# Kernel optimization log

Hardware: AMD Instinct MI355X
Metric: run time of the kernel (lower is better)

The kernel has to match this reference:

```python
import jax, jax.numpy as jnp
import numpy as np

N_NODES = 50000
N_EDGES = 800000
N_GRAPHS = 64
HIDDEN = 64


def setup_inputs() -> dict:
    key = jax.random.key(0)
    ks = jax.random.split(key, 16)
    inp = {
        "x": jax.random.normal(ks[0], (N_NODES, 1), dtype=jnp.float32),
        "edge_attr": jax.random.normal(ks[1], (N_EDGES, 1), dtype=jnp.float32),
        "edge_index": jax.random.randint(ks[2], (2, N_EDGES), 0, N_NODES, dtype=jnp.int32),
        "batch": jnp.sort(jax.random.randint(ks[3], (N_NODES,), 0, N_GRAPHS, dtype=jnp.int32)),
        # node/edge encoders: Linear(1, H)
        "W_node": jax.random.normal(ks[4], (1, HIDDEN), dtype=jnp.float32) * 0.1,
        "b_node": jnp.zeros((HIDDEN,), dtype=jnp.float32),
        "W_edge": jax.random.normal(ks[5], (1, HIDDEN), dtype=jnp.float32) * 0.1,
        "b_edge": jnp.zeros((HIDDEN,), dtype=jnp.float32),
        # message MLP: Linear(2H, H) + ReLU
        "W_msg": jax.random.normal(ks[6], (2 * HIDDEN, HIDDEN), dtype=jnp.float32) * (1.0 / np.sqrt(2 * HIDDEN)),
        "b_msg": jnp.zeros((HIDDEN,), dtype=jnp.float32),
        # update MLP: Linear(H, H) + ReLU
        "W_upd": jax.random.normal(ks[7], (HIDDEN, HIDDEN), dtype=jnp.float32) * (1.0 / np.sqrt(HIDDEN)),
        "b_upd": jnp.zeros((HIDDEN,), dtype=jnp.float32),
        # output: Linear(H, 1)
        "W_out": jax.random.normal(ks[8], (HIDDEN, 1), dtype=jnp.float32) * (1.0 / np.sqrt(HIDDEN)),
        "b_out": jnp.zeros((1,), dtype=jnp.float32),
    }
    return inp


def reference(x, edge_attr, edge_index, batch,
              W_node, b_node, W_edge, b_edge,
              W_msg, b_msg, W_upd, b_upd, W_out, b_out):
    # encoders
    h = x @ W_node + b_node                       # [N, H]
    e = edge_attr @ W_edge + b_edge               # [E, H]

    src, dst = edge_index[0], edge_index[1]
    x_j = h[src]                                  # gather source node feats [E, H]
    m = jax.nn.relu(jnp.concatenate([x_j, e], axis=-1) @ W_msg + b_msg)  # [E, H]

    # scatter-add aggregate to target nodes
    aggr = jax.ops.segment_sum(m, dst, num_segments=N_NODES)             # [N, H]

    # update MLP (applied to every node)
    upd = jax.nn.relu(aggr @ W_upd + b_upd)       # [N, H]

    # global mean pool per graph
    sums = jax.ops.segment_sum(upd, batch, num_segments=N_GRAPHS)        # [G, H]
    counts = jax.ops.segment_sum(jnp.ones((upd.shape[0],), dtype=upd.dtype), batch, num_segments=N_GRAPHS)
    avg = sums / jnp.maximum(counts, 1.0)[:, None]                       # [G, H]

    out = (avg @ W_out + b_out).squeeze(-1)       # [G]
    return out
```

## Files before the change

### kernel.cpp

```cpp
#include <hip/hip_runtime.h>

#define N_NODES 50000
#define N_EDGES 800000
#define N_GRAPHS 64
#define H 64
#define BN 64
#define NB ((N_NODES + BN - 1) / BN)
#define NGRP 8
#define CAPG 224
#define BSTRIDE (NGRP * CAPG)
#define CSTRIDE 16
#define CHUNK 4096
#define BINTHREADS 1024
#define EPT (CHUNK / BINTHREADS)
#define NCHUNK ((N_EDGES + CHUNK - 1) / CHUNK)

#define VALS_OFF  0
#define ABC_OFF   (NB * BSTRIDE * 2)
#define ZERO_OFF  (ABC_OFF + 3 * H)
#define GSUM_OFF  (ZERO_OFF)
#define GCNT_OFF  (GSUM_OFF + N_GRAPHS)
#define BCUR_OFF  (GCNT_OFF + N_GRAPHS)
#define ZERO_BYTES ((2 * N_GRAPHS + NGRP * NB * CSTRIDE) * 4)

__global__ __launch_bounds__(BINTHREADS) void k_bin(
    const float* __restrict__ x, const float* __restrict__ ea,
    const int* __restrict__ ei, int* __restrict__ bcur,
    float2* __restrict__ vals, float* __restrict__ abc,
    const float* __restrict__ Wn, const float* __restrict__ bn,
    const float* __restrict__ We, const float* __restrict__ be,
    const float* __restrict__ Wm, const float* __restrict__ bm)
{
    __shared__ int lh[NB], lbase[NB], lcur[NB];
    const int t = threadIdx.x;
    const int g = blockIdx.x & (NGRP - 1);
    for (int b = t; b < NB; b += BINTHREADS) { lh[b] = 0; lcur[b] = 0; }

    const int e0 = blockIdx.x * CHUNK;
    const int* __restrict__ src = ei;
    const int* __restrict__ dst = ei + N_EDGES;

    int   d[EPT];
    float xv[EPT], ev[EPT];
    bool  ok[EPT];
    #pragma unroll
    for (int k = 0; k < EPT; ++k) {
        const int e = e0 + t + k * BINTHREADS;
        ok[k] = (e < N_EDGES);
        const int ee = ok[k] ? e : (N_EDGES - 1);
        const int s  = src[ee];
        d[k]  = dst[ee];
        ev[k] = ea[ee];
        xv[k] = x[s];
    }
    __syncthreads();

    #pragma unroll
    for (int k = 0; k < EPT; ++k)
        if (ok[k]) atomicAdd(&lh[d[k] >> 6], 1);
    __syncthreads();

    for (int b = t; b < NB; b += BINTHREADS) {
        const int v = lh[b];
        if (v) lbase[b] = atomicAdd(&bcur[(g * NB + b) * CSTRIDE], v);
    }
    __syncthreads();

    #pragma unroll
    for (int k = 0; k < EPT; ++k) {
        if (ok[k]) {
            const int b  = d[k] >> 6;
            const int lp = atomicAdd(&lcur[b], 1);
            const int p  = lbase[b] + lp;
            if (p < CAPG) {
                const unsigned uy = (__float_as_uint(ev[k]) & 0xFFFFFFC0u) |
                                    (unsigned)(d[k] & (BN - 1));
                vals[b * BSTRIDE + g * CAPG + p] =
                    make_float2(xv[k], __uint_as_float(uy));
            }
        }
    }

    if (blockIdx.x == 0 && t < H) {
        const int k = t;
        float a = 0.f, b = 0.f, c = 0.f;
        #pragma unroll
        for (int i = 0; i < H; ++i) {
            float wt = Wm[i * H + k];
            float wb = Wm[(H + i) * H + k];
            a = fmaf(Wn[i], wt, a);
            b = fmaf(We[i], wb, b);
            c = fmaf(bn[i], wt, c);
            c = fmaf(be[i], wb, c);
        }
        abc[k]         = a;
        abc[H + k]     = b;
        abc[2 * H + k] = c + bm[k];
    }
}

__global__ __launch_bounds__(256) void k_fused(
    const float2* __restrict__ vals, const int* __restrict__ bcur,
    const float* __restrict__ abc, const float* __restrict__ Wu,
    const float* __restrict__ bu, const float* __restrict__ Wo,
    const int* __restrict__ batch,
    float* __restrict__ gsum, float* __restrict__ gcnt)
{
    __shared__ float2 stB[BSTRIDE];
    __shared__ int lh[BN], le[BN], lc[BN];
    __shared__ __align__(16) float sA[4][72];
    __shared__ float lsum[N_GRAPHS], lcnt[N_GRAPHS];

    const int t    = threadIdx.x;
    const int lane = t & 63;
    const int w    = t >> 6;
    const int b    = blockIdx.x;
    const int base = b * BSTRIDE;

    const float A   = abc[lane];
    const float B   = abc[H + lane];
    const float C   = abc[2 * H + lane];
    const float bul = bu[lane];
    const float wol = Wo[lane];
    float wr[64];
    #pragma unroll
    for (int i = 0; i < 64; ++i) wr[i] = Wu[i * H + lane];

    if (t < BN) lh[t] = 0;
    if (t < N_GRAPHS) { lsum[t] = 0.f; lcnt[t] = 0.f; }
    __syncthreads();

    int mg[NGRP];
    #pragma unroll
    for (int g = 0; g < NGRP; ++g) {
        const int v = bcur[(g * NB + b) * CSTRIDE];
        mg[g] = v < CAPG ? v : CAPG;
    }

    float2 r[NGRP];
    #pragma unroll
    for (int g = 0; g < NGRP; ++g) {
        if (t < mg[g]) {
            r[g] = vals[base + g * CAPG + t];
            atomicAdd(&lh[__float_as_uint(r[g].y) & (BN - 1)], 1);
        }
    }
    __syncthreads();

    if (t < BN) {
        const int v = lh[t];
        int incl = v;
        #pragma unroll
        for (int d = 1; d < BN; d <<= 1) {
            const int up = __shfl_up(incl, d);
            if (lane >= d) incl += up;
        }
        le[t] = incl - v;
        lc[t] = incl - v;
    }
    __syncthreads();

    #pragma unroll
    for (int g = 0; g < NGRP; ++g) {
        if (t < mg[g]) {
            const int rk = atomicAdd(&lc[__float_as_uint(r[g].y) & (BN - 1)], 1);
            stB[rk] = r[g];
        }
    }
    __syncthreads();

    #define MSG(q) fmaxf(fmaf((q).x, A, fmaf((q).y, B, C)), 0.f)
    for (int qn = 0; qn < BN / 4; ++qn) {
        const int ln   = w * (BN / 4) + qn;
        const int node = b * BN + ln;
        const int off  = le[ln];
        const int c    = lh[ln];

        float s0 = 0.f, s1 = 0.f, s2 = 0.f, s3 = 0.f;
        int j = 0;
        for (; j + 8 <= c; j += 8) {
            const float2 q0 = stB[off + j + 0], q1 = stB[off + j + 1];
            const float2 q2 = stB[off + j + 2], q3 = stB[off + j + 3];
            const float2 q4 = stB[off + j + 4], q5 = stB[off + j + 5];
            const float2 q6 = stB[off + j + 6], q7 = stB[off + j + 7];
            s0 += MSG(q0); s1 += MSG(q1); s2 += MSG(q2); s3 += MSG(q3);
            s0 += MSG(q4); s1 += MSG(q5); s2 += MSG(q6); s3 += MSG(q7);
        }
        for (; j < c; ++j) { const float2 q = stB[off + j]; s0 += MSG(q); }
        const float s = (s0 + s1) + (s2 + s3);

        sA[w][lane] = s;
        float t0 = 0.f, t1 = 0.f, t2 = 0.f, t3 = 0.f;
        #pragma unroll
        for (int i = 0; i < 64; i += 4) {
            const float4 av = *(const float4*)&sA[w][i];
            t0 = fmaf(av.x, wr[i + 0], t0);
            t1 = fmaf(av.y, wr[i + 1], t1);
            t2 = fmaf(av.z, wr[i + 2], t2);
            t3 = fmaf(av.w, wr[i + 3], t3);
        }
        const float tk = (t0 + t1) + (t2 + t3);
        float u = fmaxf(tk + bul, 0.f) * wol;
        #pragma unroll
        for (int off2 = 32; off2 > 0; off2 >>= 1)
            u += __shfl_xor(u, off2);
        if (lane == 0 && node < N_NODES) {
            const int g = batch[node];
            atomicAdd(&lsum[g], u);
            atomicAdd(&lcnt[g], 1.f);
        }
    }
    #undef MSG
    __syncthreads();
    if (t < N_GRAPHS && lcnt[t] != 0.f) {
        atomicAdd(&gsum[t], lsum[t]);
        atomicAdd(&gcnt[t], lcnt[t]);
    }
}

__global__ void k_final(const float* __restrict__ gsum,
                        const float* __restrict__ gcnt,
                        const float* __restrict__ bo,
                        float* __restrict__ out)
{
    const int g = threadIdx.x;
    if (g < N_GRAPHS)
        out[g] = gsum[g] / fmaxf(gcnt[g], 1.f) + bo[0];
}

extern "C" void kernel_launch(void* const* d_in, const int* in_sizes, int n_in,
                              void* d_out, int out_size, void* d_ws, size_t ws_size,
                              hipStream_t stream)
{
    const float* x      = (const float*)d_in[0];
    const float* ea     = (const float*)d_in[1];
    const int*   ei     = (const int*)  d_in[2];
    const int*   batch  = (const int*)  d_in[3];
    const float* Wn     = (const float*)d_in[4];
    const float* bn     = (const float*)d_in[5];
    const float* We     = (const float*)d_in[6];
    const float* be     = (const float*)d_in[7];
    const float* Wm     = (const float*)d_in[8];
    const float* bm     = (const float*)d_in[9];
    const float* Wu     = (const float*)d_in[10];
    const float* bu     = (const float*)d_in[11];
    const float* Wo     = (const float*)d_in[12];
    const float* bo     = (const float*)d_in[13];

    float*  ws   = (float*)d_ws;
    float2* vals = (float2*)(ws + VALS_OFF);
    float*  abc  = ws + ABC_OFF;
    float*  gsum = ws + GSUM_OFF;
    float*  gcnt = ws + GCNT_OFF;
    int*    bcur = (int*)(ws + BCUR_OFF);
    float*  out  = (float*)d_out;

    hipMemsetAsync(ws + ZERO_OFF, 0, ZERO_BYTES, stream);
    k_bin<<<NCHUNK, BINTHREADS, 0, stream>>>(x, ea, ei, bcur, vals, abc,
                                             Wn, bn, We, be, Wm, bm);
    k_fused<<<NB, 256, 0, stream>>>(vals, bcur, abc, Wu, bu, Wo, batch,
                                    gsum, gcnt);
    k_final<<<1, 64, 0, stream>>>(gsum, gcnt, bo, out);
}
```

Before: 57.69 us.

## Replace chunked shared-histogram binning with per-edge global atomics; batch four nodes in update

The binning kernel drops the per-block shared-memory histogram and its two-phase reservation. It now launches one thread per edge, and each thread reserves its slot with its own global atomic on the bucket counter. This removes the shared-memory passes and barriers, but raises the number of contended global atomics. The fused kernel now aggregates four nodes before running the 64x64 update matvec and the wave reductions, which is meant to improve instruction-level parallelism and cut per-node barrier and shuffle latency.

```diff
diff --git a/kernel.cpp b/kernel.cpp
--- a/kernel.cpp
+++ b/kernel.cpp
@@ -10,10 +10,7 @@
 #define CAPG 224
 #define BSTRIDE (NGRP * CAPG)
 #define CSTRIDE 16
-#define CHUNK 4096
-#define BINTHREADS 1024
-#define EPT (CHUNK / BINTHREADS)
-#define NCHUNK ((N_EDGES + CHUNK - 1) / CHUNK)
+#define NBLK_BIN ((N_EDGES + 255) / 256)
 
 #define VALS_OFF  0
 #define ABC_OFF   (NB * BSTRIDE * 2)
@@ -23,7 +20,7 @@
 #define BCUR_OFF  (GCNT_OFF + N_GRAPHS)
 #define ZERO_BYTES ((2 * N_GRAPHS + NGRP * NB * CSTRIDE) * 4)
 
-__global__ __launch_bounds__(BINTHREADS) void k_bin(
+__global__ __launch_bounds__(256) void k_bin(
     const float* __restrict__ x, const float* __restrict__ ea,
     const int* __restrict__ ei, int* __restrict__ bcur,
     float2* __restrict__ vals, float* __restrict__ abc,
@@ -31,58 +28,23 @@
     const float* __restrict__ We, const float* __restrict__ be,
     const float* __restrict__ Wm, const float* __restrict__ bm)
 {
-    __shared__ int lh[NB], lbase[NB], lcur[NB];
-    const int t = threadIdx.x;
+    const int e = blockIdx.x * 256 + threadIdx.x;
     const int g = blockIdx.x & (NGRP - 1);
-    for (int b = t; b < NB; b += BINTHREADS) { lh[b] = 0; lcur[b] = 0; }
-
-    const int e0 = blockIdx.x * CHUNK;
-    const int* __restrict__ src = ei;
-    const int* __restrict__ dst = ei + N_EDGES;
-
-    int   d[EPT];
-    float xv[EPT], ev[EPT];
-    bool  ok[EPT];
-    #pragma unroll
-    for (int k = 0; k < EPT; ++k) {
-        const int e = e0 + t + k * BINTHREADS;
-        ok[k] = (e < N_EDGES);
-        const int ee = ok[k] ? e : (N_EDGES - 1);
-        const int s  = src[ee];
-        d[k]  = dst[ee];
-        ev[k] = ea[ee];
-        xv[k] = x[s];
-    }
-    __syncthreads();
-
-    #pragma unroll
-    for (int k = 0; k < EPT; ++k)
-        if (ok[k]) atomicAdd(&lh[d[k] >> 6], 1);
-    __syncthreads();
-
-    for (int b = t; b < NB; b += BINTHREADS) {
-        const int v = lh[b];
-        if (v) lbase[b] = atomicAdd(&bcur[(g * NB + b) * CSTRIDE], v);
-    }
-    __syncthreads();
-
-    #pragma unroll
-    for (int k = 0; k < EPT; ++k) {
-        if (ok[k]) {
-            const int b  = d[k] >> 6;
-            const int lp = atomicAdd(&lcur[b], 1);
-            const int p  = lbase[b] + lp;
-            if (p < CAPG) {
-                const unsigned uy = (__float_as_uint(ev[k]) & 0xFFFFFFC0u) |
-                                    (unsigned)(d[k] & (BN - 1));
-                vals[b * BSTRIDE + g * CAPG + p] =
-                    make_float2(xv[k], __uint_as_float(uy));
-            }
-        }
-    }
-
-    if (blockIdx.x == 0 && t < H) {
-        const int k = t;
+    if (e < N_EDGES) {
+        const int   s  = ei[e];
+        const int   d  = ei[N_EDGES + e];
+        const float ev = ea[e];
+        const float xv = x[s];
+        const int   b  = d >> 6;
+        const int   p  = atomicAdd(&bcur[(g * NB + b) * CSTRIDE], 1);
+        if (p < CAPG) {
+            const unsigned uy = (__float_as_uint(ev) & 0xFFFFFFC0u) |
+                                (unsigned)(d & (BN - 1));
+            vals[b * BSTRIDE + g * CAPG + p] = make_float2(xv, __uint_as_float(uy));
+        }
+    }
+    if (blockIdx.x == 0 && threadIdx.x < H) {
+        const int k = threadIdx.x;
         float a = 0.f, b = 0.f, c = 0.f;
         #pragma unroll
         for (int i = 0; i < H; ++i) {
@@ -108,7 +70,7 @@
 {
     __shared__ float2 stB[BSTRIDE];
     __shared__ int lh[BN], le[BN], lc[BN];
-    __shared__ __align__(16) float sA[4][72];
+    __shared__ __align__(16) float sA[4][4][68];
     __shared__ float lsum[N_GRAPHS], lcnt[N_GRAPHS];
 
     const int t    = threadIdx.x;
@@ -170,46 +132,70 @@
     __syncthreads();
 
     #define MSG(q) fmaxf(fmaf((q).x, A, fmaf((q).y, B, C)), 0.f)
-    for (int qn = 0; qn < BN / 4; ++qn) {
-        const int ln   = w * (BN / 4) + qn;
-        const int node = b * BN + ln;
-        const int off  = le[ln];
-        const int c    = lh[ln];
-
-        float s0 = 0.f, s1 = 0.f, s2 = 0.f, s3 = 0.f;
-        int j = 0;
-        for (; j + 8 <= c; j += 8) {
-            const float2 q0 = stB[off + j + 0], q1 = stB[off + j + 1];
-            const float2 q2 = stB[off + j + 2], q3 = stB[off + j + 3];
-            const float2 q4 = stB[off + j + 4], q5 = stB[off + j + 5];
-            const float2 q6 = stB[off + j + 6], q7 = stB[off + j + 7];
-            s0 += MSG(q0); s1 += MSG(q1); s2 += MSG(q2); s3 += MSG(q3);
-            s0 += MSG(q4); s1 += MSG(q5); s2 += MSG(q6); s3 += MSG(q7);
-        }
-        for (; j < c; ++j) { const float2 q = stB[off + j]; s0 += MSG(q); }
-        const float s = (s0 + s1) + (s2 + s3);
-
-        sA[w][lane] = s;
-        float t0 = 0.f, t1 = 0.f, t2 = 0.f, t3 = 0.f;
+    #define AGG(LN, OUT) { \
+        const int off_ = le[LN]; const int c_ = lh[LN]; \
+        float s0 = 0.f, s1 = 0.f, s2 = 0.f, s3 = 0.f; \
+        int j = 0; \
+        for (; j + 8 <= c_; j += 8) { \
+            const float2 q0 = stB[off_ + j + 0], q1 = stB[off_ + j + 1]; \
+            const float2 q2 = stB[off_ + j + 2], q3 = stB[off_ + j + 3]; \
+            const float2 q4 = stB[off_ + j + 4], q5 = stB[off_ + j + 5]; \
+            const float2 q6 = stB[off_ + j + 6], q7 = stB[off_ + j + 7]; \
+            s0 += MSG(q0); s1 += MSG(q1); s2 += MSG(q2); s3 += MSG(q3); \
+            s0 += MSG(q4); s1 += MSG(q5); s2 += MSG(q6); s3 += MSG(q7); \
+        } \
+        for (; j < c_; ++j) { const float2 q = stB[off_ + j]; s0 += MSG(q); } \
+        OUT = (s0 + s1) + (s2 + s3); }
+
+    for (int q = 0; q < 4; ++q) {
+        const int ln0 = w * 16 + q * 4;
+        float sb0, sb1, sb2, sb3;
+        AGG(ln0 + 0, sb0);
+        AGG(ln0 + 1, sb1);
+        AGG(ln0 + 2, sb2);
+        AGG(ln0 + 3, sb3);
+        sA[w][0][lane] = sb0;
+        sA[w][1][lane] = sb1;
+        sA[w][2][lane] = sb2;
+        sA[w][3][lane] = sb3;
+
+        float p0 = 0.f, p1 = 0.f, p2 = 0.f, p3 = 0.f;
+        float q0 = 0.f, q1 = 0.f, q2 = 0.f, q3 = 0.f;
         #pragma unroll
         for (int i = 0; i < 64; i += 4) {
-            const float4 av = *(const float4*)&sA[w][i];
-            t0 = fmaf(av.x, wr[i + 0], t0);
-            t1 = fmaf(av.y, wr[i + 1], t1);
-            t2 = fmaf(av.z, wr[i + 2], t2);
-            t3 = fmaf(av.w, wr[i + 3], t3);
-        }
-        const float tk = (t0 + t1) + (t2 + t3);
-        float u = fmaxf(tk + bul, 0.f) * wol;
-        #pragma unroll
-        for (int off2 = 32; off2 > 0; off2 >>= 1)
-            u += __shfl_xor(u, off2);
-        if (lane == 0 && node < N_NODES) {
-            const int g = batch[node];
-            atomicAdd(&lsum[g], u);
-            atomicAdd(&lcnt[g], 1.f);
-        }
-    }
+            const float4 r0 = *(const float4*)&sA[w][0][i];
+            const float4 r1 = *(const float4*)&sA[w][1][i];
+            const float4 r2 = *(const float4*)&sA[w][2][i];
+            const float4 r3 = *(const float4*)&sA[w][3][i];
+            p0 = fmaf(r0.x, wr[i + 0], p0); q0 = fmaf(r0.y, wr[i + 1], q0);
+            p0 = fmaf(r0.z, wr[i + 2], p0); q0 = fmaf(r0.w, wr[i + 3], q0);
+            p1 = fmaf(r1.x, wr[i + 0], p1); q1 = fmaf(r1.y, wr[i + 1], q1);
+            p1 = fmaf(r1.z, wr[i + 2], p1); q1 = fmaf(r1.w, wr[i + 3], q1);
+            p2 = fmaf(r2.x, wr[i + 0], p2); q2 = fmaf(r2.y, wr[i + 1], q2);
+            p2 = fmaf(r2.z, wr[i + 2], p2); q2 = fmaf(r2.w, wr[i + 3], q2);
+            p3 = fmaf(r3.x, wr[i + 0], p3); q3 = fmaf(r3.y, wr[i + 1], q3);
+            p3 = fmaf(r3.z, wr[i + 2], p3); q3 = fmaf(r3.w, wr[i + 3], q3);
+        }
+        float u0 = fmaxf(p0 + q0 + bul, 0.f) * wol;
+        float u1 = fmaxf(p1 + q1 + bul, 0.f) * wol;
+        float u2 = fmaxf(p2 + q2 + bul, 0.f) * wol;
+        float u3 = fmaxf(p3 + q3 + bul, 0.f) * wol;
+        #pragma unroll
+        for (int off2 = 32; off2 > 0; off2 >>= 1) {
+            u0 += __shfl_xor(u0, off2);
+            u1 += __shfl_xor(u1, off2);
+            u2 += __shfl_xor(u2, off2);
+            u3 += __shfl_xor(u3, off2);
+        }
+        if (lane == 0) {
+            const int node0 = b * BN + ln0;
+            if (node0 + 0 < N_NODES) { atomicAdd(&lsum[batch[node0 + 0]], u0); atomicAdd(&lcnt[batch[node0 + 0]], 1.f); }
+            if (node0 + 1 < N_NODES) { atomicAdd(&lsum[batch[node0 + 1]], u1); atomicAdd(&lcnt[batch[node0 + 1]], 1.f); }
+            if (node0 + 2 < N_NODES) { atomicAdd(&lsum[batch[node0 + 2]], u2); atomicAdd(&lcnt[batch[node0 + 2]], 1.f); }
+            if (node0 + 3 < N_NODES) { atomicAdd(&lsum[batch[node0 + 3]], u3); atomicAdd(&lcnt[batch[node0 + 3]], 1.f); }
+        }
+    }
+    #undef AGG
     #undef MSG
     __syncthreads();
     if (t < N_GRAPHS && lcnt[t] != 0.f) {
@@ -256,8 +242,8 @@
     float*  out  = (float*)d_out;
 
     hipMemsetAsync(ws + ZERO_OFF, 0, ZERO_BYTES, stream);
-    k_bin<<<NCHUNK, BINTHREADS, 0, stream>>>(x, ea, ei, bcur, vals, abc,
-                                             Wn, bn, We, be, Wm, bm);
+    k_bin<<<NBLK_BIN, 256, 0, stream>>>(x, ea, ei, bcur, vals, abc,
+                                        Wn, bn, We, be, Wm, bm);
     k_fused<<<NB, 256, 0, stream>>>(vals, bcur, abc, Wu, bu, Wo, batch,
                                     gsum, gcnt);
     k_final<<<1, 64, 0, stream>>>(gsum, gcnt, bo, out);
```

Measured after the change: 79.46 us. 1.38x slower.
